# Kernel optimization log

Hardware: AMD Instinct MI355X
Metric: run time of the kernel (lower is better)

## Reference

```python
import jax, jax.numpy as jnp
import numpy as np
from jax.ops import segment_sum

NUM_GRAPHS = 1024

def setup_inputs() -> dict:
    key = jax.random.key(0)
    ks = jax.random.split(key, 10)
    N, E = 100000, 6400000
    x = jax.random.normal(ks[0], (N, 3), dtype=jnp.float32)
    edge_index = jax.random.randint(ks[1], (2, E), 0, N, dtype=jnp.int64)
    batch = jnp.sort(jax.random.randint(ks[2], (N,), 0, NUM_GRAPHS, dtype=jnp.int64))
    # GCNConv weights (glorot-ish scale) and biases
    W1 = jax.random.normal(ks[3], (3, 16), dtype=jnp.float32) * (1.0 / np.sqrt(3))
    b1 = jnp.zeros((16,), dtype=jnp.float32)
    W2 = jax.random.normal(ks[4], (16, 32), dtype=jnp.float32) * (1.0 / np.sqrt(16))
    b2 = jnp.zeros((32,), dtype=jnp.float32)
    Wl = jax.random.normal(ks[5], (32, 3), dtype=jnp.float32) * (1.0 / np.sqrt(32))
    bl = jnp.zeros((3,), dtype=jnp.float32)
    return {"x": x, "edge_index": edge_index, "batch": batch,
            "W1": W1, "b1": b1, "W2": W2, "b2": b2, "Wl": Wl, "bl": bl}

def _gcn_conv(x, src, dst, norm, W, b, num_nodes):
    # h = X W ; out[dst] += norm * h[src]  (symmetric-normalized scatter-add)
    h = x @ W                                    # [N, F_out]
    msg = h[src] * norm[:, None]                 # [E+N, F_out]
    out = segment_sum(msg, dst, num_segments=num_nodes)
    return out + b

def reference(x, edge_index, batch, W1, b1, W2, b2, Wl, bl):
    N = x.shape[0]
    # add self-loops (PyG GCNConv default)
    loops = jnp.arange(N, dtype=edge_index.dtype)
    src = jnp.concatenate([edge_index[0], loops])
    dst = jnp.concatenate([edge_index[1], loops])
    # symmetric normalization: deg over destination, norm = d^-1/2[src] * d^-1/2[dst]
    deg = segment_sum(jnp.ones_like(dst, dtype=x.dtype), dst, num_segments=N)
    dinv = jnp.where(deg > 0, jax.lax.rsqrt(deg), 0.0)
    norm = dinv[src] * dinv[dst]
    h = jax.nn.relu(_gcn_conv(x, src, dst, norm, W1, b1, N))
    h = jax.nn.relu(_gcn_conv(h, src, dst, norm, W2, b2, N))
    # global mean pool over graphs
    sums = segment_sum(h, batch, num_segments=NUM_GRAPHS)          # [G, 32]
    cnts = segment_sum(jnp.ones((N,), dtype=h.dtype), batch, num_segments=NUM_GRAPHS)
    pooled = sums / jnp.maximum(cnts, 1.0)[:, None]
    return pooled @ Wl + bl
```

## Files before the change

kernel.cpp:

```cpp
#include <hip/hip_runtime.h>
#include <hip/hip_fp16.h>

#define NG 1024
#define SCAN_B 1024
#define BSH2 9
#define GN 512
#define MAXBIN 256
#define NB2 256
#define SCB 1024
#define TSZ 8192
#define PGR 64

__global__ void k_zero(float* __restrict__ pooled, float* __restrict__ cnt) {
    int i = blockIdx.x * blockDim.x + threadIdx.x;
    if (i < NG * 32) pooled[i] = 0.0f;
    if (i < NG) cnt[i] = 0.0f;
}

__global__ void k_scanA(const int* __restrict__ in, int* __restrict__ tmp,
                        int* __restrict__ part, int L) {
    __shared__ int s[SCAN_B];
    int gid = blockIdx.x * SCAN_B + threadIdx.x;
    s[threadIdx.x] = (gid < L) ? in[gid] : 0;
    __syncthreads();
    for (int off = 1; off < SCAN_B; off <<= 1) {
        int t = (threadIdx.x >= off) ? s[threadIdx.x - off] : 0;
        __syncthreads();
        s[threadIdx.x] += t;
        __syncthreads();
    }
    if (gid < L) tmp[gid] = s[threadIdx.x];
    if (threadIdx.x == SCAN_B - 1) part[blockIdx.x] = s[SCAN_B - 1];
}

__global__ void k_scanB(int* __restrict__ part, int NB) {
    __shared__ int s[SCAN_B];
    int v = (threadIdx.x < NB) ? part[threadIdx.x] : 0;
    s[threadIdx.x] = v;
    __syncthreads();
    for (int off = 1; off < SCAN_B; off <<= 1) {
        int t = (threadIdx.x >= off) ? s[threadIdx.x - off] : 0;
        __syncthreads();
        s[threadIdx.x] += t;
        __syncthreads();
    }
    if (threadIdx.x < NB) part[threadIdx.x] = threadIdx.x ? s[threadIdx.x - 1] : 0;
}

__global__ void k_applyT(const int* __restrict__ tmp2, const int* __restrict__ part2,
                         int* __restrict__ histT, int L) {
    int k = blockIdx.x * blockDim.x + threadIdx.x;
    if (k < L) {
        int incl = tmp2[k] + part2[k >> 10];
        int orig = histT[k];
        histT[k] = incl - orig;
        if (k == L - 1) histT[L] = incl;
    }
}

__global__ __launch_bounds__(SCB) void k_hist(const int* __restrict__ dst,
                                              int* __restrict__ histT,
                                              int E, int CH, int NBIN) {
    __shared__ int cnt_s[MAXBIN];
    if (threadIdx.x < MAXBIN) cnt_s[threadIdx.x] = 0;
    __syncthreads();
    int blk = blockIdx.x;
    int s0 = blk * CH, s1 = s0 + CH; if (s1 > E) s1 = E;
    for (int e = s0 + threadIdx.x; e < s1; e += SCB)
        atomicAdd(&cnt_s[dst[e] >> BSH2], 1);
    __syncthreads();
    for (int b = threadIdx.x; b < NBIN; b += SCB)
        histT[b * NB2 + blk] = cnt_s[b];
}

__global__ __launch_bounds__(1024) void k_scatter(const int* __restrict__ src,
                                                  const int* __restrict__ dst,
                                                  const int* __restrict__ offT,
                                                  unsigned* __restrict__ binned,
                                                  int E, int CH, int NBIN) {
    __shared__ unsigned stg[TSZ];
    __shared__ unsigned char sbin[TSZ];
    __shared__ int th[MAXBIN];
    __shared__ int sc[MAXBIN];
    __shared__ int toff[MAXBIN + 1];
    __shared__ int gcur[MAXBIN];
    int tid = threadIdx.x;
    int blk = blockIdx.x;
    if (tid < MAXBIN) {
        th[tid] = 0;
        gcur[tid] = (tid < NBIN) ? offT[tid * NB2 + blk] : 0;
    }
    __syncthreads();
    int s0 = blk * CH, s1 = s0 + CH; if (s1 > E) s1 = E;
    for (int t0 = s0; t0 < s1; t0 += TSZ) {
        int cnt = s1 - t0; if (cnt > TSZ) cnt = TSZ;
        unsigned pk[8]; int rk[8]; int bn[8];
#pragma unroll
        for (int j = 0; j < 8; ++j) {
            int e = t0 + tid + j * 1024;
            bn[j] = -1;
            if (e < t0 + cnt) {
                int d = dst[e];
                int b = d >> BSH2;
                pk[j] = (unsigned)src[e] | ((unsigned)(d & (GN - 1)) << 17);
                bn[j] = b;
                rk[j] = atomicAdd(&th[b], 1);
            }
        }
        __syncthreads();
        if (tid < MAXBIN) sc[tid] = th[tid];
        __syncthreads();
        for (int off = 1; off < MAXBIN; off <<= 1) {
            int v = 0;
            if (tid < MAXBIN && tid >= off) v = sc[tid - off];
            __syncthreads();
            if (tid < MAXBIN) sc[tid] += v;
            __syncthreads();
        }
        if (tid < MAXBIN) toff[tid + 1] = sc[tid];
        if (tid == 0) toff[0] = 0;
        __syncthreads();
#pragma unroll
        for (int j = 0; j < 8; ++j)
            if (bn[j] >= 0) {
                int p = toff[bn[j]] + rk[j];
                stg[p] = pk[j];
                sbin[p] = (unsigned char)bn[j];
            }
        __syncthreads();
        for (int i = tid; i < cnt; i += 1024) {
            int b = sbin[i];
            binned[gcur[b] + (i - toff[b])] = stg[i];
        }
        __syncthreads();
        if (tid < MAXBIN) { gcur[tid] += th[tid]; th[tid] = 0; }
        __syncthreads();
    }
}

__global__ __launch_bounds__(1024) void k_csr3(
        const unsigned* __restrict__ binned, const int* __restrict__ offT,
        int* __restrict__ row_ptr, float* __restrict__ dinv,
        int* __restrict__ csr, int N, int NBIN) {
    __shared__ int cnt[GN];
    __shared__ int pre[GN];
    __shared__ int cur[GN];
    int tid = threadIdx.x;
    int b = blockIdx.x;
    int base = offT[b * NB2];
    int end  = offT[(b + 1) * NB2];
    if (tid < GN) cnt[tid] = 0;
    __syncthreads();
    for (int i = base + tid; i < end; i += 1024)
        atomicAdd(&cnt[(binned[i] >> 17) & (GN - 1)], 1);
    __syncthreads();
    if (tid < GN) pre[tid] = cnt[tid];
    __syncthreads();
    for (int off = 1; off < GN; off <<= 1) {
        int v = 0;
        if (tid < GN && tid >= off) v = pre[tid - off];
        __syncthreads();
        if (tid < GN) pre[tid] += v;
        __syncthreads();
    }
    int gv = (b << BSH2) + tid;
    if (tid < GN) {
        int ex = pre[tid] - cnt[tid];
        pre[tid] = ex;
        cur[tid] = 0;
        if (gv < N) {
            row_ptr[gv] = base + ex;
            dinv[gv] = rsqrtf((float)cnt[tid] + 1.0f);
        }
    }
    if (b == NBIN - 1 && tid == 0) row_ptr[N] = end;
    __syncthreads();
    for (int i = base + tid; i < end; i += 1024) {
        unsigned p = binned[i];
        int dl = (int)((p >> 17) & (GN - 1));
        int pos = atomicAdd(&cur[dl], 1);
        csr[base + pre[dl] + pos] = (int)(p & 0x1FFFFu);
    }
}

__global__ void k_xd(const float* __restrict__ x, const float* __restrict__ dinv,
                     float4* __restrict__ xd, int N) {
    int v = blockIdx.x * blockDim.x + threadIdx.x;
    if (v >= N) return;
    float d = dinv[v];
    xd[v] = make_float4(d * x[v * 3 + 0], d * x[v * 3 + 1], d * x[v * 3 + 2], 0.0f);
}

__global__ __launch_bounds__(256) void k_ga(const int* __restrict__ row_ptr,
                                            const int* __restrict__ csr,
                                            const float4* __restrict__ xd,
                                            const float* __restrict__ dinv,
                                            const float* __restrict__ W1,
                                            const float* __restrict__ b1,
                                            __half* __restrict__ g1h, int N) {
    __shared__ float sW[48];
    __shared__ float sb[16];
    if (threadIdx.x < 48) sW[threadIdx.x] = W1[threadIdx.x];
    if (threadIdx.x < 16) sb[threadIdx.x] = b1[threadIdx.x];
    __syncthreads();
    int t = blockIdx.x * blockDim.x + threadIdx.x;
    int v = t >> 3, l = t & 7;
    if (v >= N) return;
    int beg = row_ptr[v], end = row_ptr[v + 1];
    float sx = 0.0f, sy = 0.0f, sz = 0.0f;
#pragma unroll 4
    for (int e = beg + l; e < end; e += 8) {
        float4 a = xd[csr[e]];
        sx += a.x; sy += a.y; sz += a.z;
    }
    sx += __shfl_xor(sx, 1, 64); sy += __shfl_xor(sy, 1, 64); sz += __shfl_xor(sz, 1, 64);
    sx += __shfl_xor(sx, 2, 64); sy += __shfl_xor(sy, 2, 64); sz += __shfl_xor(sz, 2, 64);
    sx += __shfl_xor(sx, 4, 64); sy += __shfl_xor(sy, 4, 64); sz += __shfl_xor(sz, 4, 64);
    float4 self = xd[v];
    sx += self.x; sy += self.y; sz += self.z;
    float d = dinv[v];
    int f0 = l * 2;
    float h0 = fmaxf(d * (sx * sW[f0]     + sy * sW[16 + f0]     + sz * sW[32 + f0])     + sb[f0],     0.0f);
    float h1 = fmaxf(d * (sx * sW[f0 + 1] + sy * sW[16 + f0 + 1] + sz * sW[32 + f0 + 1]) + sb[f0 + 1], 0.0f);
    __half2 p = __halves2half2(__float2half(d * h0), __float2half(d * h1));
    *(unsigned*)(g1h + (size_t)v * 16 + f0) = *(unsigned*)&p;
}

__global__ __launch_bounds__(256) void k_gb(const int* __restrict__ row_ptr,
                                            const int* __restrict__ csr,
                                            const __half* __restrict__ g1h,
                                            const float* __restrict__ dinv,
                                            const float* __restrict__ W2,
                                            const float* __restrict__ b2,
                                            const int* __restrict__ batch,
                                            float* __restrict__ pooled,
                                            float* __restrict__ cnt, int N) {
    __shared__ float sW[512];
    __shared__ float sb[32];
    __shared__ float sacc[PGR * 32];
    __shared__ int   scnt[PGR];
    __shared__ int   sgf;
    int t = threadIdx.x;
    for (int i = t; i < 512; i += 256) sW[i] = W2[i];
    if (t < 32) sb[t] = b2[t];
    for (int i = t; i < PGR * 32; i += 256) sacc[i] = 0.0f;
    if (t < PGR) scnt[t] = 0;
    int v0 = blockIdx.x * 16;
    if (t == 0) sgf = (v0 < N) ? batch[v0] : 0;
    __syncthreads();
    int gt = blockIdx.x * blockDim.x + t;
    int v = gt >> 4, l = gt & 15;
    int gfirst = sgf;
    if (v < N) {
        int fh = l & 1, ep = l >> 1;
        const char* gbase = (const char*)g1h + fh * 16;
        float s8[8] = {0.f, 0.f, 0.f, 0.f, 0.f, 0.f, 0.f, 0.f};
        int beg = row_ptr[v], end = row_ptr[v + 1];
#pragma unroll 4
        for (int e = beg + ep; e < end; e += 8) {
            int s = csr[e];
            uint4 raw = *(const uint4*)(gbase + (size_t)s * 32);
            float2 f0 = __half22float2(*(__half2*)&raw.x);
            float2 f1 = __half22float2(*(__half2*)&raw.y);
            float2 f2 = __half22float2(*(__half2*)&raw.z);
            float2 f3 = __half22float2(*(__half2*)&raw.w);
            s8[0] += f0.x; s8[1] += f0.y; s8[2] += f1.x; s8[3] += f1.y;
            s8[4] += f2.x; s8[5] += f2.y; s8[6] += f3.x; s8[7] += f3.y;
        }
        if (ep == 0) {
            uint4 raw = *(const uint4*)(gbase + (size_t)v * 32);
            float2 f0 = __half22float2(*(__half2*)&raw.x);
            float2 f1 = __half22float2(*(__half2*)&raw.y);
            float2 f2 = __half22float2(*(__half2*)&raw.z);
            float2 f3 = __half22float2(*(__half2*)&raw.w);
            s8[0] += f0.x; s8[1] += f0.y; s8[2] += f1.x; s8[3] += f1.y;
            s8[4] += f2.x; s8[5] += f2.y; s8[6] += f3.x; s8[7] += f3.y;
        }
#pragma unroll
        for (int j = 0; j < 8; ++j) {
            s8[j] += __shfl_xor(s8[j], 2, 64);
            s8[j] += __shfl_xor(s8[j], 4, 64);
            s8[j] += __shfl_xor(s8[j], 8, 64);
        }
        float o8[8];
#pragma unroll
        for (int j = 0; j < 8; ++j) o8[j] = __shfl_xor(s8[j], 1, 64);
        float t16[16];
        if (fh == 0) {
#pragma unroll
            for (int j = 0; j < 8; ++j) { t16[j] = s8[j]; t16[8 + j] = o8[j]; }
        } else {
#pragma unroll
            for (int j = 0; j < 8; ++j) { t16[j] = o8[j]; t16[8 + j] = s8[j]; }
        }
        float d = dinv[v];
        int g = batch[v];
        int gl = g - gfirst;
        int f0 = l * 2;
#pragma unroll
        for (int j = 0; j < 2; ++j) {
            float acc = 0.0f;
#pragma unroll
            for (int k = 0; k < 16; ++k) acc += t16[k] * sW[k * 32 + f0 + j];
            float h = fmaxf(d * acc + sb[f0 + j], 0.0f);
            if (gl < PGR) atomicAdd(&sacc[gl * 32 + f0 + j], h);
            else          atomicAdd(&pooled[g * 32 + f0 + j], h);
        }
        if (l == 0) {
            if (gl < PGR) atomicAdd(&scnt[gl], 1);
            else          atomicAdd(&cnt[g], 1.0f);
        }
    }
    __syncthreads();
    for (int i = t; i < PGR * 32; i += 256) {
        float val = sacc[i];
        if (val != 0.0f) atomicAdd(&pooled[(gfirst + (i >> 5)) * 32 + (i & 31)], val);
    }
    for (int i = t; i < PGR; i += 256) {
        int c = scnt[i];
        if (c) atomicAdd(&cnt[gfirst + i], (float)c);
    }
}

__global__ void k_out(const float* __restrict__ pooled, const float* __restrict__ cnt,
                      const float* __restrict__ Wl, const float* __restrict__ bl,
                      float* __restrict__ out) {
    int t = blockIdx.x * blockDim.x + threadIdx.x;
    if (t >= NG * 3) return;
    int g = t / 3, c = t % 3;
    float inv = 1.0f / fmaxf(cnt[g], 1.0f);
    float s = bl[c];
#pragma unroll
    for (int f = 0; f < 32; ++f) s += pooled[g * 32 + f] * inv * Wl[f * 3 + c];
    out[g * 3 + c] = s;
}

extern "C" void kernel_launch(void* const* d_in, const int* in_sizes, int n_in,
                              void* d_out, int out_size, void* d_ws, size_t ws_size,
                              hipStream_t stream) {
    const float* x     = (const float*)d_in[0];
    const int*   ei    = (const int*)d_in[1];
    const int*   batch = (const int*)d_in[2];
    const float* W1    = (const float*)d_in[3];
    const float* b1    = (const float*)d_in[4];
    const float* W2    = (const float*)d_in[5];
    const float* b2    = (const float*)d_in[6];
    const float* Wl    = (const float*)d_in[7];
    const float* bl    = (const float*)d_in[8];

    const int N = in_sizes[0] / 3;
    const int E = in_sizes[1] / 2;
    const int* src = ei;
    const int* dst = ei + E;
    const int NBIN = (N + GN - 1) >> BSH2;
    const int CH   = (E + NB2 - 1) / NB2;
    const int L    = NBIN * NB2;

    char* w = (char*)d_ws;
    int*      row_ptr = (int*)w;      w += (size_t)(N + 4) * 4;
    float*    dinv    = (float*)w;    w += (size_t)N * 4;
    int*      histT   = (int*)w;      w += (size_t)(L + 4) * 4;
    int*      tmp2    = (int*)w;      w += (size_t)L * 4;
    int*      part2   = (int*)w;      w += (size_t)SCAN_B * 4;
    unsigned* binned  = (unsigned*)w; w += (size_t)(E + 16) * 4;
    int*      csr     = (int*)w;      w += (size_t)E * 4;
    float4*   xd      = (float4*)w;   w += (size_t)N * 16;
    __half*   g1h     = (__half*)w;   w += ((size_t)N * 32 + 15) & ~(size_t)15;
    float*    pooled  = (float*)w;    w += (size_t)NG * 32 * 4;
    float*    cnt     = (float*)w;    w += (size_t)NG * 4;

    const int B = 256;
    const int gN  = (N + B - 1) / B;
    const int NBl = (L + SCAN_B - 1) / SCAN_B;

    k_zero<<<(NG * 32 + B - 1) / B, B, 0, stream>>>(pooled, cnt);

    k_hist<<<NB2, SCB, 0, stream>>>(dst, histT, E, CH, NBIN);
    k_scanA<<<NBl, SCAN_B, 0, stream>>>(histT, tmp2, part2, L);
    k_scanB<<<1, SCAN_B, 0, stream>>>(part2, NBl);
    k_applyT<<<(L + B - 1) / B, B, 0, stream>>>(tmp2, part2, histT, L);
    k_scatter<<<NB2, 1024, 0, stream>>>(src, dst, histT, binned, E, CH, NBIN);
    k_csr3<<<NBIN, 1024, 0, stream>>>(binned, histT, row_ptr, dinv, csr, N, NBIN);

    k_xd<<<gN, B, 0, stream>>>(x, dinv, xd, N);
    k_ga<<<((size_t)N * 8 + B - 1) / B, B, 0, stream>>>(row_ptr, csr, xd, dinv, W1, b1, g1h, N);
    k_gb<<<((size_t)N * 16 + B - 1) / B, B, 0, stream>>>(row_ptr, csr, g1h, dinv, W2, b2, batch,
                                                         pooled, cnt, N);
    k_out<<<(NG * 3 + B - 1) / B, B, 0, stream>>>(pooled, cnt, Wl, bl, (float*)d_out);
}
```

Measured before the change: 192.7 us.

## Fuse zero/xd kernels into neighbors and remap layer-2 gather to 8 lanes per node

Folds the pooled/count zeroing into k_applyT and the xd scaling into k_csr3, which removes two kernel launches. k_gb now uses 8 lanes per node, each loading the full 32-byte fp16 row, instead of 16 lanes each loading half a row. This cuts shuffle work and the extra half-exchange step, but doubles per-lane register accumulators. Unroll pragmas are also added in k_scatter and k_ga.

```diff
diff --git a/kernel.cpp b/kernel.cpp
--- a/kernel.cpp
+++ b/kernel.cpp
@@ -11,12 +11,6 @@
 #define TSZ 8192
 #define PGR 64
 
-__global__ void k_zero(float* __restrict__ pooled, float* __restrict__ cnt) {
-    int i = blockIdx.x * blockDim.x + threadIdx.x;
-    if (i < NG * 32) pooled[i] = 0.0f;
-    if (i < NG) cnt[i] = 0.0f;
-}
-
 __global__ void k_scanA(const int* __restrict__ in, int* __restrict__ tmp,
                         int* __restrict__ part, int L) {
     __shared__ int s[SCAN_B];
@@ -48,7 +42,8 @@
 }
 
 __global__ void k_applyT(const int* __restrict__ tmp2, const int* __restrict__ part2,
-                         int* __restrict__ histT, int L) {
+                         int* __restrict__ histT, int L,
+                         float* __restrict__ pooled, float* __restrict__ cnt) {
     int k = blockIdx.x * blockDim.x + threadIdx.x;
     if (k < L) {
         int incl = tmp2[k] + part2[k >> 10];
@@ -56,6 +51,8 @@
         histT[k] = incl - orig;
         if (k == L - 1) histT[L] = incl;
     }
+    if (k < NG * 32) pooled[k] = 0.0f;
+    if (k < NG) cnt[k] = 0.0f;
 }
 
 __global__ __launch_bounds__(SCB) void k_hist(const int* __restrict__ dst,
@@ -128,6 +125,7 @@
                 sbin[p] = (unsigned char)bn[j];
             }
         __syncthreads();
+#pragma unroll 4
         for (int i = tid; i < cnt; i += 1024) {
             int b = sbin[i];
             binned[gcur[b] + (i - toff[b])] = stg[i];
@@ -141,6 +139,7 @@
 __global__ __launch_bounds__(1024) void k_csr3(
         const unsigned* __restrict__ binned, const int* __restrict__ offT,
         int* __restrict__ row_ptr, float* __restrict__ dinv,
+        const float* __restrict__ x, float4* __restrict__ xd,
         int* __restrict__ csr, int N, int NBIN) {
     __shared__ int cnt[GN];
     __shared__ int pre[GN];
@@ -170,7 +169,10 @@
         cur[tid] = 0;
         if (gv < N) {
             row_ptr[gv] = base + ex;
-            dinv[gv] = rsqrtf((float)cnt[tid] + 1.0f);
+            float d = rsqrtf((float)cnt[tid] + 1.0f);
+            dinv[gv] = d;
+            xd[gv] = make_float4(d * x[gv * 3 + 0], d * x[gv * 3 + 1],
+                                 d * x[gv * 3 + 2], 0.0f);
         }
     }
     if (b == NBIN - 1 && tid == 0) row_ptr[N] = end;
@@ -181,14 +183,6 @@
         int pos = atomicAdd(&cur[dl], 1);
         csr[base + pre[dl] + pos] = (int)(p & 0x1FFFFu);
     }
-}
-
-__global__ void k_xd(const float* __restrict__ x, const float* __restrict__ dinv,
-                     float4* __restrict__ xd, int N) {
-    int v = blockIdx.x * blockDim.x + threadIdx.x;
-    if (v >= N) return;
-    float d = dinv[v];
-    xd[v] = make_float4(d * x[v * 3 + 0], d * x[v * 3 + 1], d * x[v * 3 + 2], 0.0f);
 }
 
 __global__ __launch_bounds__(256) void k_ga(const int* __restrict__ row_ptr,
@@ -208,7 +202,7 @@
     if (v >= N) return;
     int beg = row_ptr[v], end = row_ptr[v + 1];
     float sx = 0.0f, sy = 0.0f, sz = 0.0f;
-#pragma unroll 4
+#pragma unroll 8
     for (int e = beg + l; e < end; e += 8) {
         float4 a = xd[csr[e]];
         sx += a.x; sy += a.y; sz += a.z;
@@ -245,63 +239,61 @@
     if (t < 32) sb[t] = b2[t];
     for (int i = t; i < PGR * 32; i += 256) sacc[i] = 0.0f;
     if (t < PGR) scnt[t] = 0;
-    int v0 = blockIdx.x * 16;
+    int v0 = blockIdx.x * 32;
     if (t == 0) sgf = (v0 < N) ? batch[v0] : 0;
     __syncthreads();
     int gt = blockIdx.x * blockDim.x + t;
-    int v = gt >> 4, l = gt & 15;
+    int v = gt >> 3, l = gt & 7;
     int gfirst = sgf;
     if (v < N) {
-        int fh = l & 1, ep = l >> 1;
-        const char* gbase = (const char*)g1h + fh * 16;
-        float s8[8] = {0.f, 0.f, 0.f, 0.f, 0.f, 0.f, 0.f, 0.f};
+        const uint4* g4 = (const uint4*)g1h;
+        float s16[16];
+#pragma unroll
+        for (int j = 0; j < 16; ++j) s16[j] = 0.0f;
         int beg = row_ptr[v], end = row_ptr[v + 1];
 #pragma unroll 4
-        for (int e = beg + ep; e < end; e += 8) {
+        for (int e = beg + l; e < end; e += 8) {
             int s = csr[e];
-            uint4 raw = *(const uint4*)(gbase + (size_t)s * 32);
-            float2 f0 = __half22float2(*(__half2*)&raw.x);
-            float2 f1 = __half22float2(*(__half2*)&raw.y);
-            float2 f2 = __half22float2(*(__half2*)&raw.z);
-            float2 f3 = __half22float2(*(__half2*)&raw.w);
-            s8[0] += f0.x; s8[1] += f0.y; s8[2] += f1.x; s8[3] += f1.y;
-            s8[4] += f2.x; s8[5] += f2.y; s8[6] += f3.x; s8[7] += f3.y;
-        }
-        if (ep == 0) {
-            uint4 raw = *(const uint4*)(gbase + (size_t)v * 32);
-            float2 f0 = __half22float2(*(__half2*)&raw.x);
-            float2 f1 = __half22float2(*(__half2*)&raw.y);
-            float2 f2 = __half22float2(*(__half2*)&raw.z);
-            float2 f3 = __half22float2(*(__half2*)&raw.w);
-            s8[0] += f0.x; s8[1] += f0.y; s8[2] += f1.x; s8[3] += f1.y;
-            s8[4] += f2.x; s8[5] += f2.y; s8[6] += f3.x; s8[7] += f3.y;
-        }
-#pragma unroll
-        for (int j = 0; j < 8; ++j) {
-            s8[j] += __shfl_xor(s8[j], 2, 64);
-            s8[j] += __shfl_xor(s8[j], 4, 64);
-            s8[j] += __shfl_xor(s8[j], 8, 64);
-        }
-        float o8[8];
-#pragma unroll
-        for (int j = 0; j < 8; ++j) o8[j] = __shfl_xor(s8[j], 1, 64);
-        float t16[16];
-        if (fh == 0) {
-#pragma unroll
-            for (int j = 0; j < 8; ++j) { t16[j] = s8[j]; t16[8 + j] = o8[j]; }
-        } else {
-#pragma unroll
-            for (int j = 0; j < 8; ++j) { t16[j] = o8[j]; t16[8 + j] = s8[j]; }
+            uint4 lo = g4[(size_t)s * 2];
+            uint4 hi = g4[(size_t)s * 2 + 1];
+            float2 f;
+            f = __half22float2(*(__half2*)&lo.x); s16[0]  += f.x; s16[1]  += f.y;
+            f = __half22float2(*(__half2*)&lo.y); s16[2]  += f.x; s16[3]  += f.y;
+            f = __half22float2(*(__half2*)&lo.z); s16[4]  += f.x; s16[5]  += f.y;
+            f = __half22float2(*(__half2*)&lo.w); s16[6]  += f.x; s16[7]  += f.y;
+            f = __half22float2(*(__half2*)&hi.x); s16[8]  += f.x; s16[9]  += f.y;
+            f = __half22float2(*(__half2*)&hi.y); s16[10] += f.x; s16[11] += f.y;
+            f = __half22float2(*(__half2*)&hi.z); s16[12] += f.x; s16[13] += f.y;
+            f = __half22float2(*(__half2*)&hi.w); s16[14] += f.x; s16[15] += f.y;
+        }
+        if (l == 0) {
+            uint4 lo = g4[(size_t)v * 2];
+            uint4 hi = g4[(size_t)v * 2 + 1];
+            float2 f;
+            f = __half22float2(*(__half2*)&lo.x); s16[0]  += f.x; s16[1]  += f.y;
+            f = __half22float2(*(__half2*)&lo.y); s16[2]  += f.x; s16[3]  += f.y;
+            f = __half22float2(*(__half2*)&lo.z); s16[4]  += f.x; s16[5]  += f.y;
+            f = __half22float2(*(__half2*)&lo.w); s16[6]  += f.x; s16[7]  += f.y;
+            f = __half22float2(*(__half2*)&hi.x); s16[8]  += f.x; s16[9]  += f.y;
+            f = __half22float2(*(__half2*)&hi.y); s16[10] += f.x; s16[11] += f.y;
+            f = __half22float2(*(__half2*)&hi.z); s16[12] += f.x; s16[13] += f.y;
+            f = __half22float2(*(__half2*)&hi.w); s16[14] += f.x; s16[15] += f.y;
+        }
+#pragma unroll
+        for (int j = 0; j < 16; ++j) {
+            s16[j] += __shfl_xor(s16[j], 1, 64);
+            s16[j] += __shfl_xor(s16[j], 2, 64);
+            s16[j] += __shfl_xor(s16[j], 4, 64);
         }
         float d = dinv[v];
         int g = batch[v];
         int gl = g - gfirst;
-        int f0 = l * 2;
-#pragma unroll
-        for (int j = 0; j < 2; ++j) {
+        int f0 = l * 4;
+#pragma unroll
+        for (int j = 0; j < 4; ++j) {
             float acc = 0.0f;
 #pragma unroll
-            for (int k = 0; k < 16; ++k) acc += t16[k] * sW[k * 32 + f0 + j];
+            for (int k = 0; k < 16; ++k) acc += s16[k] * sW[k * 32 + f0 + j];
             float h = fmaxf(d * acc + sb[f0 + j], 0.0f);
             if (gl < PGR) atomicAdd(&sacc[gl * 32 + f0 + j], h);
             else          atomicAdd(&pooled[g * 32 + f0 + j], h);
@@ -370,21 +362,17 @@
     float*    cnt     = (float*)w;    w += (size_t)NG * 4;
 
     const int B = 256;
-    const int gN  = (N + B - 1) / B;
     const int NBl = (L + SCAN_B - 1) / SCAN_B;
-
-    k_zero<<<(NG * 32 + B - 1) / B, B, 0, stream>>>(pooled, cnt);
 
     k_hist<<<NB2, SCB, 0, stream>>>(dst, histT, E, CH, NBIN);
     k_scanA<<<NBl, SCAN_B, 0, stream>>>(histT, tmp2, part2, L);
     k_scanB<<<1, SCAN_B, 0, stream>>>(part2, NBl);
-    k_applyT<<<(L + B - 1) / B, B, 0, stream>>>(tmp2, part2, histT, L);
+    k_applyT<<<(L + B - 1) / B, B, 0, stream>>>(tmp2, part2, histT, L, pooled, cnt);
     k_scatter<<<NB2, 1024, 0, stream>>>(src, dst, histT, binned, E, CH, NBIN);
-    k_csr3<<<NBIN, 1024, 0, stream>>>(binned, histT, row_ptr, dinv, csr, N, NBIN);
-
-    k_xd<<<gN, B, 0, stream>>>(x, dinv, xd, N);
+    k_csr3<<<NBIN, 1024, 0, stream>>>(binned, histT, row_ptr, dinv, x, xd, csr, N, NBIN);
+
     k_ga<<<((size_t)N * 8 + B - 1) / B, B, 0, stream>>>(row_ptr, csr, xd, dinv, W1, b1, g1h, N);
-    k_gb<<<((size_t)N * 16 + B - 1) / B, B, 0, stream>>>(row_ptr, csr, g1h, dinv, W2, b2, batch,
-                                                         pooled, cnt, N);
+    k_gb<<<((size_t)N * 8 + B - 1) / B, B, 0, stream>>>(row_ptr, csr, g1h, dinv, W2, b2, batch,
+                                                        pooled, cnt, N);
     k_out<<<(NG * 3 + B - 1) / B, B, 0, stream>>>(pooled, cnt, Wl, bl, (float*)d_out);
 }
```

Result: faster. 183.6 us (-4.7%).
